# Kernel tuning notes

Hardware: AMD Instinct MI355X
Metric: run time of the kernel (lower is better)

The kernel has to match this reference:

```python
import jax, jax.numpy as jnp
import numpy as np

N_USER = 100_000
N_WALLET = 100_000
E = 1_600_000
HID, OUT = 128, 64
H, C = 4, 32  # GAT heads, per-head channels (HID // 4)
U_IN, W_IN = 16, 4
EPS = 1e-5


def _sage(x_src, x_dst, ei, w_l, b_l, w_r):
    """PyG SAGEConv (mean aggr): lin_l(mean_j x_j) + lin_r(x_i)."""
    src, dst = ei[0], ei[1]
    n = x_dst.shape[0]
    s = jax.ops.segment_sum(x_src[src], dst, num_segments=n)
    deg = jax.ops.segment_sum(jnp.ones((src.shape[0],), x_src.dtype), dst, num_segments=n)
    agg = s / jnp.maximum(deg, 1.0)[:, None]
    return agg @ w_l + b_l + x_dst @ w_r


def _bn(x, g, b):
    """BatchNorm over node dim (training-mode batch stats)."""
    m = x.mean(0)
    v = x.var(0)
    return (x - m) * jax.lax.rsqrt(v + EPS) * g + b


def _segment_softmax(logits, seg, n):
    m = jax.ops.segment_max(logits, seg, num_segments=n)
    e = jnp.exp(logits - m[seg])
    s = jax.ops.segment_sum(e, seg, num_segments=n)
    return e / (s[seg] + 1e-16)


def _gat(x, ei, w, a_src, a_dst, bias):
    """PyG GATConv with self-loops, heads concatenated. Dropout off (eval)."""
    n = x.shape[0]
    loop = jnp.arange(n, dtype=ei.dtype)
    src = jnp.concatenate([ei[0], loop])
    dst = jnp.concatenate([ei[1], loop])
    xp = (x @ w).reshape(n, H, C)                      # [n,H,C]
    al_s = (xp * a_src).sum(-1)                        # [n,H]
    al_d = (xp * a_dst).sum(-1)                        # [n,H]
    logits = jax.nn.leaky_relu(al_s[src] + al_d[dst], 0.2)  # [E+n,H]
    alpha = _segment_softmax(logits, dst, n)
    out = jax.ops.segment_sum(xp[src] * alpha[:, :, None], dst, num_segments=n)
    return out.reshape(n, H * C) + bias


def setup_inputs() -> dict:
    key = jax.random.key(0)
    ks = jax.random.split(key, 24)
    rn = lambda k, s, sc=0.05: jax.random.normal(k, s, jnp.float32) * sc
    ei = lambda k, n: jax.random.randint(k, (2, E), 0, n, jnp.int32)
    return {
        "x_user": rn(ks[0], (N_USER, U_IN), 1.0),
        "x_wallet": rn(ks[1], (N_WALLET, W_IN), 1.0),
        "w_u2w_l": rn(ks[2], (U_IN, HID)), "b_u2w": jnp.zeros((HID,), jnp.float32), "w_u2w_r": rn(ks[3], (W_IN, HID)),
        "w_w2u_l": rn(ks[4], (W_IN, HID)), "b_w2u": jnp.zeros((HID,), jnp.float32), "w_w2u_r": rn(ks[5], (U_IN, HID)),
        "w_u2u_l": rn(ks[6], (U_IN, HID)), "b_u2u": jnp.zeros((HID,), jnp.float32), "w_u2u_r": rn(ks[7], (U_IN, HID)),
        "bn_u_g": jnp.ones((HID,), jnp.float32), "bn_u_b": jnp.zeros((HID,), jnp.float32),
        "bn_w_g": jnp.ones((HID,), jnp.float32), "bn_w_b": jnp.zeros((HID,), jnp.float32),
        "gat_w": rn(ks[8], (HID, H * C)), "gat_as": rn(ks[9], (H, C)), "gat_ad": rn(ks[10], (H, C)),
        "gat_b": jnp.zeros((HID,), jnp.float32),
        "bn2_g": jnp.ones((HID,), jnp.float32), "bn2_b": jnp.zeros((HID,), jnp.float32),
        "proj_w": rn(ks[11], (HID, OUT)), "proj_b": jnp.zeros((OUT,), jnp.float32),
        "ei_uw": ei(ks[12], N_USER),   # src user -> dst wallet (both 100k)
        "ei_wu": ei(ks[13], N_WALLET),  # src wallet -> dst user
        "ei_uu": ei(ks[14], N_USER),
    }


def reference(x_user, x_wallet, w_u2w_l, b_u2w, w_u2w_r, w_w2u_l, b_w2u, w_w2u_r,
              w_u2u_l, b_u2u, w_u2u_r, bn_u_g, bn_u_b, bn_w_g, bn_w_b,
              gat_w, gat_as, gat_ad, gat_b, bn2_g, bn2_b, proj_w, proj_b,
              ei_uw, ei_wu, ei_uu):
    h_w_from_u = jax.nn.relu(_sage(x_user, x_wallet, ei_uw, w_u2w_l, b_u2w, w_u2w_r))
    h_u_from_w = jax.nn.relu(_sage(x_wallet, x_user, ei_wu, w_w2u_l, b_w2u, w_w2u_r))
    h_u_from_u = jax.nn.relu(_sage(x_user, x_user, ei_uu, w_u2u_l, b_u2u, w_u2u_r))
    h_user = _bn(h_u_from_w + h_u_from_u, bn_u_g, bn_u_b)
    _ = _bn(h_w_from_u, bn_w_g, bn_w_b)  # h_wallet: computed in torch module but unused in output
    h_user = jax.nn.relu(_gat(h_user, ei_uu, gat_w, gat_as, gat_ad, gat_b))
    h_user = _bn(h_user, bn2_g, bn2_b)
    return jax.nn.relu(h_user @ proj_w + proj_b)  # dropout = identity (eval)
```

## Files before the change

kernel.cpp:

```cpp
#include <hip/hip_runtime.h>
#include <hip/hip_bf16.h>
#include <cstdint>
#include <cstddef>

#define NN   100000
#define NE   1600000
#define CAP  48

#define NBKT 98
#define BSH  10
#define FB   48
#define BCAP 17408
#define ACHUNK 2048
#define NABLK 784
#define SUBSH 7

#define NTILES 1563
#define CH_BN 500

typedef __attribute__((ext_vector_type(8))) short short8;
typedef __attribute__((ext_vector_type(4))) float floatx4;

__device__ inline short f2bs(float x) {
    __hip_bfloat16 h = __float2bfloat16(x);
    return *reinterpret_cast<short*>(&h);
}
__device__ inline int pack2(float a, float b) {
    return ((int)(unsigned short)f2bs(b) << 16) | (unsigned short)f2bs(a);
}
__device__ inline float bflo(unsigned p) { return __uint_as_float(p << 16); }
__device__ inline float bfhi(unsigned p) { return __uint_as_float(p & 0xFFFF0000u); }

#define OFF_PRE   ((size_t)0)
#define OFF_BKTU  ((size_t)0)
#define OFF_BKTW  ((size_t)1705984)
#define OFF_XP    ((size_t)12800000)
#define OFF_COLU  ((size_t)19200000)
#define OFF_CNTU  ((size_t)25600000)
#define OFF_CNTW  ((size_t)25700000)
#define OFF_BCUR  ((size_t)25800000)
#define OFF_S1    ((size_t)25800256)
#define OFF_Q1    ((size_t)25800384)
#define OFF_S2    ((size_t)25800512)
#define OFF_Q2    ((size_t)25800640)
#define OFF_ALS   ((size_t)25801280)
#define OFF_ALD   ((size_t)26201280)
#define OFF_AGGU  ((size_t)26601280)
#define OFF_AGGW  ((size_t)28201280)
#define ZBASE     OFF_BCUR
#define ZFLOATS   ((size_t)768)

__global__ void __launch_bounds__(256) bin_edges(
    const int* __restrict__ ei_u, const int* __restrict__ ei_w,
    int* __restrict__ bcur_u, int* __restrict__ bkt_u,
    int* __restrict__ bcur_w, int* __restrict__ bkt_w) {
    const int* ei = blockIdx.y ? ei_w : ei_u;
    int* bcur = blockIdx.y ? bcur_w : bcur_u;
    int* bkt  = blockIdx.y ? bkt_w  : bkt_u;
    __shared__ int lcnt[NBKT];
    __shared__ int lbuf[NBKT * FB];
    for (int i = threadIdx.x; i < NBKT; i += 256) lcnt[i] = 0;
    __syncthreads();
    int base = blockIdx.x * ACHUNK;
    #pragma unroll
    for (int k = 0; k < ACHUNK / 256; k++) {
        int e = base + k * 256 + threadIdx.x;
        if (e < NE) {
            int src = ei[e], dst = ei[NE + e];
            int b = dst >> BSH;
            int pk = ((dst & ((1 << BSH) - 1)) << 17) | src;
            int pos = atomicAdd(&lcnt[b], 1);
            if (pos < FB) lbuf[b * FB + pos] = pk;
            else {
                int g = atomicAdd(&bcur[b], 1);
                if (g < BCAP) bkt[(size_t)b * BCAP + g] = pk;
            }
        }
    }
    __syncthreads();
    int wid = threadIdx.x >> 6, lane = threadIdx.x & 63;
    const int BPW = (NBKT + 3) / 4;
    int b0w = wid * BPW;
    int nb = NBKT - b0w; if (nb > BPW) nb = BPW;
    int myn = 0, myg = 0;
    if (lane < nb) {
        int c = lcnt[b0w + lane];
        myn = c < FB ? c : FB;
        if (myn > 0) myg = atomicAdd(&bcur[b0w + lane], myn);
    }
    for (int j = 0; j < nb; j++) {
        int n = __shfl(myn, j, 64);
        if (n == 0) continue;
        int g0 = __shfl(myg, j, 64);
        int b = b0w + j;
        if (lane < n) {
            int g = g0 + lane;
            if (g < BCAP) bkt[(size_t)b * BCAP + g] = lbuf[b * FB + lane];
        }
    }
}

__global__ void __launch_bounds__(256) csr_from_buckets(
    const int* __restrict__ bcur_u, const int* __restrict__ bkt_u,
    int* __restrict__ cntg_u, int* __restrict__ colg_u,
    const int* __restrict__ bcur_w, const int* __restrict__ bkt_w,
    int* __restrict__ cntg_w, int* __restrict__ colg_w) {
    const int* bcur = blockIdx.y ? bcur_w : bcur_u;
    const int* bkt  = blockIdx.y ? bkt_w  : bkt_u;
    int* cnt_g = blockIdx.y ? cntg_w : cntg_u;
    int* col_g = blockIdx.y ? colg_w : colg_u;
    int B = blockIdx.x >> 3, sub = blockIdx.x & 7;
    int node_base = (B << BSH) + (sub << SUBSH);
    if (node_base >= NN) return;
    __shared__ int cnt[128];
    __shared__ int col[128 * CAP];
    if (threadIdx.x < 128) cnt[threadIdx.x] = 0;
    __syncthreads();
    int n = bcur[B]; if (n > BCAP) n = BCAP;
    const int* bp = bkt + (size_t)B * BCAP;
    for (int i = threadIdx.x; i < n; i += 256) {
        int p = bp[i];
        int dlow = p >> 17;
        if ((dlow >> SUBSH) == sub) {
            int d = dlow & 127;
            int pos = atomicAdd(&cnt[d], 1);
            if (pos < CAP) col[d * CAP + pos] = p & 0x1FFFF;
        }
    }
    __syncthreads();
    int nn_here = NN - node_base; if (nn_here > 128) nn_here = 128;
    if (threadIdx.x < nn_here) cnt_g[node_base + threadIdx.x] = cnt[threadIdx.x];
    int total4 = nn_here * CAP / 4;
    const int4* cs = (const int4*)col;
    int4* cg = (int4*)(col_g + (size_t)node_base * CAP);
    for (int i = threadIdx.x; i < total4; i += 256) cg[i] = cs[i];
}

__global__ void __launch_bounds__(256) sage_gather(
    const float* __restrict__ xu, const float* __restrict__ xw,
    const int* __restrict__ cnt_u, const int* __restrict__ col_u,
    const int* __restrict__ cnt_w, const int* __restrict__ col_w,
    float* __restrict__ aggu, float* __restrict__ aggw) {
    int i = (blockIdx.x * 256 + threadIdx.x) >> 6;
    int lane = threadIdx.x & 63;

    int degu = cnt_u[i], degw = cnt_w[i];
    int nu = degu < CAP ? degu : CAP, nw = degw < CAP ? degw : CAP;
    int mycu = (lane < nu) ? col_u[(size_t)i * CAP + lane] : 0;
    int mycw = (lane < nw) ? col_w[(size_t)i * CAP + lane] : 0;

    float vu;
    {
        int j = lane >> 4, k = lane & 15;
        float v0 = 0.f, v1 = 0.f, v2 = 0.f, v3 = 0.f;
        int iters = (nu + 15) >> 4;
        for (int it = 0; it < iters; it++) {
            int bb = j + (it << 4);
            int s0 = __shfl(mycu, bb, 64);
            int s1 = __shfl(mycu, bb + 4, 64);
            int s2 = __shfl(mycu, bb + 8, 64);
            int s3 = __shfl(mycu, bb + 12, 64);
            float x0 = xu[(size_t)s0 * 16 + k];
            float x1 = xu[(size_t)s1 * 16 + k];
            float x2 = xu[(size_t)s2 * 16 + k];
            float x3 = xu[(size_t)s3 * 16 + k];
            if (bb < nu)      v0 += x0;
            if (bb + 4 < nu)  v1 += x1;
            if (bb + 8 < nu)  v2 += x2;
            if (bb + 12 < nu) v3 += x3;
        }
        float v = (v0 + v1) + (v2 + v3);
        v += __shfl_xor(v, 16, 64);
        v += __shfl_xor(v, 32, 64);
        vu = v;
    }
    float vw;
    {
        int j = lane >> 2, k = lane & 3;
        float v0 = 0.f, v1 = 0.f;
        int iters = (nw + 31) >> 5;
        for (int it = 0; it < iters; it++) {
            int b0 = j + (it << 5), b1 = b0 + 16;
            int s0 = __shfl(mycw, b0, 64);
            int s1 = __shfl(mycw, b1, 64);
            float x0 = xw[(size_t)s0 * 4 + k];
            float x1 = xw[(size_t)s1 * 4 + k];
            if (b0 < nw) v0 += x0;
            if (b1 < nw) v1 += x1;
        }
        float v = v0 + v1;
        v += __shfl_xor(v, 4, 64);
        v += __shfl_xor(v, 8, 64);
        v += __shfl_xor(v, 16, 64);
        v += __shfl_xor(v, 32, 64);
        vw = v;
    }
    float iu = 1.f / fmaxf((float)degu, 1.f);
    float iw = 1.f / fmaxf((float)degw, 1.f);
    if (lane < 16) aggu[(size_t)i * 16 + lane] = vu * iu;
    if (lane < 4)  aggw[(size_t)i * 4 + lane]  = vw * iw;
}

__global__ void __launch_bounds__(256, 2) sage_gemm(
    const float* __restrict__ aggu, const float* __restrict__ aggw,
    const float* __restrict__ xu,
    const float* __restrict__ wl_w2u, const float* __restrict__ b_w2u, const float* __restrict__ wr_w2u,
    const float* __restrict__ wl_u2u, const float* __restrict__ b_u2u, const float* __restrict__ wr_u2u,
    __hip_bfloat16* __restrict__ pre) {
    __shared__ short lw[16 * 64 * 8];
    __shared__ short la[64 * 136];
    int tid = threadIdx.x;
    for (int idx = tid; idx < 8192; idx += 256) {
        int mat = idx >> 12;
        int k = (idx >> 7) & 31, n = idx & 127;
        float w;
        if (mat == 0)
            w = (k < 4) ? wl_w2u[k * 128 + n] : (k < 20 ? wr_w2u[(k - 4) * 128 + n] : 0.f);
        else
            w = (k < 16) ? wl_u2u[k * 128 + n] : wr_u2u[(k - 16) * 128 + n];
        int t = n >> 4, l15 = n & 15, q = (k >> 3) & 3, j = k & 7;
        lw[((mat * 8 + t) * 64 + q * 16 + l15) * 8 + j] = f2bs(w);
    }
    __syncthreads();
    int wv = tid >> 6, lane = tid & 63;
    int quad = lane >> 4, l15 = lane & 15;
    short8 w1[8], w2[8];
    #pragma unroll
    for (int t = 0; t < 8; t++) {
        w1[t] = *(const short8*)&lw[(t * 64 + lane) * 8];
        w2[t] = *(const short8*)&lw[((8 + t) * 64 + lane) * 8];
    }
    float bw[8], bu[8];
    #pragma unroll
    for (int t = 0; t < 8; t++) {
        bw[t] = b_w2u[t * 16 + l15];
        bu[t] = b_u2u[t * 16 + l15];
    }
    for (int tile = blockIdx.x; tile < NTILES; tile += gridDim.x) {
        int nbase = tile * 64;
        __syncthreads();
        {
            int node = tid >> 2, p = tid & 3;
            int gn = nbase + node;
            float4 v = make_float4(0.f, 0.f, 0.f, 0.f);
            if (gn < NN) v = *(const float4*)&xu[(size_t)gn * 16 + 4 * p];
            int2 pk; pk.x = pack2(v.x, v.y); pk.y = pack2(v.z, v.w);
            *(int2*)&la[node * 136 + 4 + 4 * p] = pk;
            *(int2*)&la[node * 136 + 48 + 4 * p] = pk;
        }
        {
            int node = tid >> 2, p = tid & 3;
            int gn = nbase + node;
            float4 v = make_float4(0.f, 0.f, 0.f, 0.f);
            if (gn < NN) v = *(const float4*)&aggu[(size_t)gn * 16 + 4 * p];
            int2 pk; pk.x = pack2(v.x, v.y); pk.y = pack2(v.z, v.w);
            *(int2*)&la[node * 136 + 32 + 4 * p] = pk;
        }
        if (tid < 64) {
            int node = tid, gn = nbase + node;
            float4 v = make_float4(0.f, 0.f, 0.f, 0.f);
            if (gn < NN) v = *(const float4*)&aggw[(size_t)gn * 4];
            int2 pk; pk.x = pack2(v.x, v.y); pk.y = pack2(v.z, v.w);
            *(int2*)&la[node * 136 + 0] = pk;
            int2 z; z.x = 0; z.y = 0;
            *(int2*)&la[node * 136 + 20] = z;
            *(int2*)&la[node * 136 + 24] = z;
            *(int2*)&la[node * 136 + 28] = z;
        }
        __syncthreads();
        short8 af1 = *(const short8*)&la[(wv * 16 + l15) * 136 + quad * 8];
        short8 af2 = *(const short8*)&la[(wv * 16 + l15) * 136 + 32 + quad * 8];
        floatx4 acc1[8], acc2[8];
        #pragma unroll
        for (int t = 0; t < 8; t++) {
            acc1[t] = (floatx4){0.f, 0.f, 0.f, 0.f};
            acc2[t] = (floatx4){0.f, 0.f, 0.f, 0.f};
        }
        #pragma unroll
        for (int t = 0; t < 8; t++) {
            acc1[t] = __builtin_amdgcn_mfma_f32_16x16x32_bf16(af1, w1[t], acc1[t], 0, 0, 0);
            acc2[t] = __builtin_amdgcn_mfma_f32_16x16x32_bf16(af2, w2[t], acc2[t], 0, 0, 0);
        }
        __syncthreads();
        #pragma unroll
        for (int t = 0; t < 8; t++)
            #pragma unroll
            for (int r = 0; r < 4; r++) {
                float v1 = fmaxf(acc1[t][r] + bw[t], 0.f);
                float v2 = fmaxf(acc2[t][r] + bu[t], 0.f);
                la[(wv * 16 + quad * 4 + r) * 136 + t * 16 + l15] = f2bs(v1 + v2);
            }
        __syncthreads();
        #pragma unroll
        for (int c = 0; c < 4; c++) {
            int idx = c * 256 + tid;
            int node = idx >> 4, f8 = (idx & 15) * 8;
            int gn = nbase + node;
            if (gn < NN)
                *(int4*)(pre + (size_t)gn * 128 + f8) = *(const int4*)&la[node * 136 + f8];
        }
    }
}

__global__ void __launch_bounds__(256) bn_stats_pre2(const unsigned* __restrict__ x2,
                                                     float* __restrict__ sum, float* __restrict__ sq) {
    int f2 = threadIdx.x & 63, half = threadIdx.x >> 6;
    int n0 = blockIdx.x * CH_BN;
    float s0 = 0.f, q0 = 0.f, s1 = 0.f, q1 = 0.f;
    for (int i = n0 + half; i < n0 + CH_BN; i += 4) {
        unsigned p = x2[(size_t)i * 64 + f2];
        float v0 = bflo(p), v1 = bfhi(p);
        s0 += v0; q0 += v0 * v0; s1 += v1; q1 += v1 * v1;
    }
    __shared__ float a0[256], c0[256], a1[256], c1[256];
    a0[threadIdx.x] = s0; c0[threadIdx.x] = q0;
    a1[threadIdx.x] = s1; c1[threadIdx.x] = q1;
    __syncthreads();
    if (half == 0) {
        for (int h = 1; h < 4; h++) {
            s0 += a0[h * 64 + f2]; q0 += c0[h * 64 + f2];
            s1 += a1[h * 64 + f2]; q1 += c1[h * 64 + f2];
        }
        atomicAdd(&sum[2 * f2], s0);     atomicAdd(&sq[2 * f2], q0);
        atomicAdd(&sum[2 * f2 + 1], s1); atomicAdd(&sq[2 * f2 + 1], q1);
    }
}

__global__ void __launch_bounds__(256) bn_stats_act2(const unsigned* __restrict__ x2,
                                                     const float* __restrict__ gb,
                                                     float* __restrict__ sum, float* __restrict__ sq) {
    int f2 = threadIdx.x & 63, half = threadIdx.x >> 6;
    int n0 = blockIdx.x * CH_BN;
    float gb0 = gb[2 * f2], gb1 = gb[2 * f2 + 1];
    float s0 = 0.f, q0 = 0.f, s1 = 0.f, q1 = 0.f;
    for (int i = n0 + half; i < n0 + CH_BN; i += 4) {
        unsigned p = x2[(size_t)i * 64 + f2];
        float v0 = fmaxf(bflo(p) + gb0, 0.f), v1 = fmaxf(bfhi(p) + gb1, 0.f);
        s0 += v0; q0 += v0 * v0; s1 += v1; q1 += v1 * v1;
    }
    __shared__ float a0[256], c0[256], a1[256], c1[256];
    a0[threadIdx.x] = s0; c0[threadIdx.x] = q0;
    a1[threadIdx.x] = s1; c1[threadIdx.x] = q1;
    __syncthreads();
    if (half == 0) {
        for (int h = 1; h < 4; h++) {
            s0 += a0[h * 64 + f2]; q0 += c0[h * 64 + f2];
            s1 += a1[h * 64 + f2]; q1 += c1[h * 64 + f2];
        }
        atomicAdd(&sum[2 * f2], s0);     atomicAdd(&sq[2 * f2], q0);
        atomicAdd(&sum[2 * f2 + 1], s1); atomicAdd(&sq[2 * f2 + 1], q1);
    }
}

__global__ void __launch_bounds__(256, 2) gemm_al(
    const unsigned* __restrict__ pre2, const float* __restrict__ s1, const float* __restrict__ q1,
    const float* __restrict__ bng, const float* __restrict__ bnb,
    const float* __restrict__ gw, const float* __restrict__ gas, const float* __restrict__ gad,
    __hip_bfloat16* __restrict__ xp, float* __restrict__ al_s, float* __restrict__ al_d) {
    __shared__ short lw[32 * 64 * 8];
    __shared__ short la[64 * 136];
    __shared__ float lsc[128], lsh[128];
    int tid = threadIdx.x;
    if (tid < 128) {
        float m = s1[tid] * (1.0f / NN);
        float v = q1[tid] * (1.0f / NN) - m * m;
        float sc = bng[tid] * rsqrtf(v + 1e-5f);
        lsc[tid] = sc; lsh[tid] = bnb[tid] - m * sc;
    }
    for (int idx = tid; idx < 16384; idx += 256) {
        int k = idx >> 7, n = idx & 127;
        int t = n >> 4, l15 = n & 15, s = k >> 5, q = (k >> 3) & 3, j = k & 7;
        lw[(((t * 4 + s) * 64) + q * 16 + l15) * 8 + j] = f2bs(gw[idx]);
    }
    __syncthreads();
    int wv = tid >> 6, lane = tid & 63;
    int quad = lane >> 4, l15 = lane & 15;
    short8 wfrag[8][4];
    #pragma unroll
    for (int t = 0; t < 8; t++)
        #pragma unroll
        for (int s = 0; s < 4; s++)
            wfrag[t][s] = *(const short8*)&lw[((t * 4 + s) * 64 + lane) * 8];
    float asv[8], adv[8];
    #pragma unroll
    for (int t = 0; t < 8; t++) {
        asv[t] = gas[t * 16 + l15];
        adv[t] = gad[t * 16 + l15];
    }
    for (int tile = blockIdx.x; tile < NTILES; tile += gridDim.x) {
        int nbase = tile * 64;
        __syncthreads();
        #pragma unroll
        for (int c = 0; c < 8; c++) {
            int idx = c * 256 + tid;
            int node = idx >> 5, g = idx & 31;
            uint2 pp = make_uint2(0u, 0u);
            int gn = nbase + node;
            if (gn < NN) pp = *(const uint2*)&pre2[(size_t)gn * 64 + 2 * g];
            int f = 4 * g;
            float v0 = bflo(pp.x), v1 = bfhi(pp.x), v2 = bflo(pp.y), v3 = bfhi(pp.y);
            int2 pk;
            pk.x = pack2(v0 * lsc[f] + lsh[f],         v1 * lsc[f + 1] + lsh[f + 1]);
            pk.y = pack2(v2 * lsc[f + 2] + lsh[f + 2], v3 * lsc[f + 3] + lsh[f + 3]);
            *(int2*)&la[node * 136 + f] = pk;
        }
        __syncthreads();
        short8 af[4];
        #pragma unroll
        for (int s = 0; s < 4; s++)
            af[s] = *(const short8*)&la[(wv * 16 + l15) * 136 + s * 32 + quad * 8];
        floatx4 acc[8];
        #pragma unroll
        for (int t = 0; t < 8; t++) acc[t] = (floatx4){0.f, 0.f, 0.f, 0.f};
        #pragma unroll
        for (int s = 0; s < 4; s++)
            #pragma unroll
            for (int t = 0; t < 8; t++)
                acc[t] = __builtin_amdgcn_mfma_f32_16x16x32_bf16(af[s], wfrag[t][s], acc[t], 0, 0, 0);
        #pragma unroll
        for (int r = 0; r < 4; r++) {
            int node = nbase + wv * 16 + quad * 4 + r;
            #pragma unroll
            for (int h = 0; h < 4; h++) {
                float vs = acc[2 * h][r] * asv[2 * h] + acc[2 * h + 1][r] * asv[2 * h + 1];
                float vd = acc[2 * h][r] * adv[2 * h] + acc[2 * h + 1][r] * adv[2 * h + 1];
                #pragma unroll
                for (int m = 8; m >= 1; m >>= 1) {
                    vs += __shfl_xor(vs, m, 64);
                    vd += __shfl_xor(vd, m, 64);
                }
                if (l15 == 0 && node < NN) {
                    al_s[(size_t)node * 4 + h] = vs;
                    al_d[(size_t)node * 4 + h] = vd;
                }
            }
        }
        __syncthreads();
        #pragma unroll
        for (int t = 0; t < 8; t++)
            #pragma unroll
            for (int r = 0; r < 4; r++)
                la[(wv * 16 + quad * 4 + r) * 136 + t * 16 + l15] = f2bs(acc[t][r]);
        __syncthreads();
        #pragma unroll
        for (int c = 0; c < 4; c++) {
            int idx = c * 256 + tid;
            int node = idx >> 4, f8 = (idx & 15) * 8;
            int gn = nbase + node;
            if (gn < NN)
                *(int4*)(xp + (size_t)gn * 128 + f8) = *(const int4*)&la[node * 136 + f8];
        }
    }
}

__global__ void __launch_bounds__(256, 2) gemm_proj(
    const unsigned* __restrict__ gat2, const float* __restrict__ gb,
    const float* __restrict__ s2, const float* __restrict__ q2,
    const float* __restrict__ bng, const float* __restrict__ bnb,
    const float* __restrict__ pw, const float* __restrict__ pb,
    float* __restrict__ out) {
    __shared__ short lw[16 * 64 * 8];
    __shared__ short la[64 * 136];
    __shared__ float lsc[128], lsh[128], lgb[128];
    int tid = threadIdx.x;
    if (tid < 128) {
        float m = s2[tid] * (1.0f / NN);
        float v = q2[tid] * (1.0f / NN) - m * m;
        float sc = bng[tid] * rsqrtf(v + 1e-5f);
        lsc[tid] = sc; lsh[tid] = bnb[tid] - m * sc;
        lgb[tid] = gb[tid];
    }
    for (int idx = tid; idx < 8192; idx += 256) {
        int k = idx >> 6, n = idx & 63;
        int t = n >> 4, l15 = n & 15, s = k >> 5, q = (k >> 3) & 3, j = k & 7;
        lw[(((t * 4 + s) * 64) + q * 16 + l15) * 8 + j] = f2bs(pw[idx]);
    }
    __syncthreads();
    int wv = tid >> 6, lane = tid & 63;
    int quad = lane >> 4, l15 = lane & 15;
    short8 wfrag[4][4];
    #pragma unroll
    for (int t = 0; t < 4; t++)
        #pragma unroll
        for (int s = 0; s < 4; s++)
            wfrag[t][s] = *(const short8*)&lw[((t * 4 + s) * 64 + lane) * 8];
    float pbv[4];
    #pragma unroll
    for (int t = 0; t < 4; t++) pbv[t] = pb[t * 16 + l15];
    for (int tile = blockIdx.x; tile < NTILES; tile += gridDim.x) {
        int nbase = tile * 64;
        __syncthreads();
        #pragma unroll
        for (int c = 0; c < 8; c++) {
            int idx = c * 256 + tid;
            int node = idx >> 5, g = idx & 31;
            uint2 pp = make_uint2(0u, 0u);
            int gn = nbase + node;
            if (gn < NN) pp = *(const uint2*)&gat2[(size_t)gn * 64 + 2 * g];
            int f = 4 * g;
            float h0 = fmaxf(bflo(pp.x) + lgb[f],     0.f) * lsc[f]     + lsh[f];
            float h1 = fmaxf(bfhi(pp.x) + lgb[f + 1], 0.f) * lsc[f + 1] + lsh[f + 1];
            float h2 = fmaxf(bflo(pp.y) + lgb[f + 2], 0.f) * lsc[f + 2] + lsh[f + 2];
            float h3 = fmaxf(bfhi(pp.y) + lgb[f + 3], 0.f) * lsc[f + 3] + lsh[f + 3];
            int2 pk; pk.x = pack2(h0, h1); pk.y = pack2(h2, h3);
            *(int2*)&la[node * 136 + f] = pk;
        }
        __syncthreads();
        short8 af[4];
        #pragma unroll
        for (int s = 0; s < 4; s++)
            af[s] = *(const short8*)&la[(wv * 16 + l15) * 136 + s * 32 + quad * 8];
        floatx4 acc[4];
        #pragma unroll
        for (int t = 0; t < 4; t++) acc[t] = (floatx4){0.f, 0.f, 0.f, 0.f};
        #pragma unroll
        for (int s = 0; s < 4; s++)
            #pragma unroll
            for (int t = 0; t < 4; t++)
                acc[t] = __builtin_amdgcn_mfma_f32_16x16x32_bf16(af[s], wfrag[t][s], acc[t], 0, 0, 0);
        #pragma unroll
        for (int r = 0; r < 4; r++) {
            int gn = nbase + wv * 16 + quad * 4 + r;
            if (gn < NN) {
                #pragma unroll
                for (int t = 0; t < 4; t++)
                    out[(size_t)gn * 64 + t * 16 + l15] = fmaxf(acc[t][r] + pbv[t], 0.f);
            }
        }
    }
}

__global__ void __launch_bounds__(256) gat_gather(
    const int* __restrict__ cnt_u, const int* __restrict__ col_u,
    const float* __restrict__ al_s, const float* __restrict__ al_d,
    const unsigned* __restrict__ xp2, unsigned* __restrict__ gout2) {
    int i = (blockIdx.x * 256 + threadIdx.x) >> 6;
    int lane = threadIdx.x & 63;
    int h = lane >> 4;
    float ad = al_d[(size_t)i * 4 + h];
    int deg = cnt_u[i];
    int n = deg < CAP ? deg : CAP;
    int mycol = (lane < n) ? col_u[(size_t)i * CAP + lane] : 0;
    float l = al_s[(size_t)i * 4 + h] + ad; l = l > 0.f ? l : 0.2f * l;
    float e = __expf(l);
    unsigned p = xp2[(size_t)i * 64 + lane];
    float acc0 = e * bflo(p), acc1 = e * bfhi(p), den = e;
    int b = 0;
    for (; b + 4 <= n; b += 4) {
        int s0 = __shfl(mycol, b, 64);
        int s1 = __shfl(mycol, b + 1, 64);
        int s2 = __shfl(mycol, b + 2, 64);
        int s3 = __shfl(mycol, b + 3, 64);
        float a0 = al_s[(size_t)s0 * 4 + h];
        float a1 = al_s[(size_t)s1 * 4 + h];
        float a2 = al_s[(size_t)s2 * 4 + h];
        float a3 = al_s[(size_t)s3 * 4 + h];
        unsigned p0 = xp2[(size_t)s0 * 64 + lane];
        unsigned p1 = xp2[(size_t)s1 * 64 + lane];
        unsigned p2 = xp2[(size_t)s2 * 64 + lane];
        unsigned p3 = xp2[(size_t)s3 * 64 + lane];
        float l0 = a0 + ad; l0 = l0 > 0.f ? l0 : 0.2f * l0;
        float l1 = a1 + ad; l1 = l1 > 0.f ? l1 : 0.2f * l1;
        float l2 = a2 + ad; l2 = l2 > 0.f ? l2 : 0.2f * l2;
        float l3 = a3 + ad; l3 = l3 > 0.f ? l3 : 0.2f * l3;
        float e0 = __expf(l0), e1 = __expf(l1), e2 = __expf(l2), e3 = __expf(l3);
        acc0 += e0 * bflo(p0) + e1 * bflo(p1) + e2 * bflo(p2) + e3 * bflo(p3);
        acc1 += e0 * bfhi(p0) + e1 * bfhi(p1) + e2 * bfhi(p2) + e3 * bfhi(p3);
        den  += e0 + e1 + e2 + e3;
    }
    for (; b < n; b++) {
        int s = __shfl(mycol, b, 64);
        float a = al_s[(size_t)s * 4 + h];
        unsigned pp = xp2[(size_t)s * 64 + lane];
        float ll = a + ad; ll = ll > 0.f ? ll : 0.2f * ll;
        float ee = __expf(ll);
        acc0 += ee * bflo(pp);
        acc1 += ee * bfhi(pp);
        den += ee;
    }
    float r = 1.0f / (den + 1e-16f);
    gout2[(size_t)i * 64 + lane] = (unsigned)pack2(acc0 * r, acc1 * r);
}

extern "C" void kernel_launch(void* const* d_in, const int* in_sizes, int n_in,
                              void* d_out, int out_size, void* d_ws, size_t ws_size,
                              hipStream_t stream) {
    const float* x_user   = (const float*)d_in[0];
    const float* x_wallet = (const float*)d_in[1];
    const float* w_w2u_l  = (const float*)d_in[5];
    const float* b_w2u    = (const float*)d_in[6];
    const float* w_w2u_r  = (const float*)d_in[7];
    const float* w_u2u_l  = (const float*)d_in[8];
    const float* b_u2u    = (const float*)d_in[9];
    const float* w_u2u_r  = (const float*)d_in[10];
    const float* bn_u_g   = (const float*)d_in[11];
    const float* bn_u_b   = (const float*)d_in[12];
    const float* gat_w    = (const float*)d_in[15];
    const float* gat_as   = (const float*)d_in[16];
    const float* gat_ad   = (const float*)d_in[17];
    const float* gat_b    = (const float*)d_in[18];
    const float* bn2_g    = (const float*)d_in[19];
    const float* bn2_b    = (const float*)d_in[20];
    const float* proj_w   = (const float*)d_in[21];
    const float* proj_b   = (const float*)d_in[22];
    const int* ei_wu      = (const int*)d_in[24];
    const int* ei_uu      = (const int*)d_in[25];
    float* out = (float*)d_out;
    float* ws  = (float*)d_ws;

    __hip_bfloat16* pre = (__hip_bfloat16*)(ws + OFF_PRE);
    unsigned* pre2 = (unsigned*)(ws + OFF_PRE);
    int*   bkt_u  = (int*)(ws + OFF_BKTU);
    int*   bkt_w  = (int*)(ws + OFF_BKTW);
    __hip_bfloat16* xp = (__hip_bfloat16*)(ws + OFF_XP);
    unsigned* xp2 = (unsigned*)(ws + OFF_XP);
    int*   col_w  = (int*)(ws + OFF_XP);
    int*   col_u  = (int*)(ws + OFF_COLU);
    int*   cnt_u  = (int*)(ws + OFF_CNTU);
    int*   cnt_w  = (int*)(ws + OFF_CNTW);
    int*   bcur_u = (int*)(ws + OFF_BCUR);
    int*   bcur_w = (int*)(ws + OFF_BCUR) + 128;
    float* al_s = ws + OFF_ALS, *al_d = ws + OFF_ALD;
    float* s1 = ws + OFF_S1, *q1 = ws + OFF_Q1;
    float* s2 = ws + OFF_S2, *q2 = ws + OFF_Q2;
    float* aggu = ws + OFF_AGGU, *aggw = ws + OFF_AGGW;

    hipMemsetAsync(ws + ZBASE, 0, ZFLOATS * sizeof(float), stream);

    bin_edges<<<dim3(NABLK, 2), 256, 0, stream>>>(ei_uu, ei_wu, bcur_u, bkt_u, bcur_w, bkt_w);
    csr_from_buckets<<<dim3(NBKT * 8, 2), 256, 0, stream>>>(
        bcur_u, bkt_u, cnt_u, col_u, bcur_w, bkt_w, cnt_w, col_w);

    sage_gather<<<NN / 4, 256, 0, stream>>>(
        x_user, x_wallet, cnt_u, col_u, cnt_w, col_w, aggu, aggw);

    sage_gemm<<<512, 256, 0, stream>>>(
        aggu, aggw, x_user, w_w2u_l, b_w2u, w_w2u_r, w_u2u_l, b_u2u, w_u2u_r, pre);

    bn_stats_pre2<<<NN / CH_BN, 256, 0, stream>>>(pre2, s1, q1);

    gemm_al<<<512, 256, 0, stream>>>(pre2, s1, q1, bn_u_g, bn_u_b,
                                     gat_w, gat_as, gat_ad, xp, al_s, al_d);

    unsigned* gat2 = pre2;
    gat_gather<<<NN / 4, 256, 0, stream>>>(cnt_u, col_u, al_s, al_d, xp2, gat2);

    bn_stats_act2<<<NN / CH_BN, 256, 0, stream>>>(gat2, gat_b, s2, q2);

    gemm_proj<<<512, 256, 0, stream>>>(gat2, gat_b, s2, q2, bn2_g, bn2_b,
                                       proj_w, proj_b, out);
}
```

Measured before the change: 495.0 us.

## Fuse CSR construction with SAGE mean aggregation and use exp2 in GAT softmax

Merges the CSR-building kernel and the SAGE neighbour gather into one kernel that aggregates directly from the CSR columns held in shared memory. The wallet CSR no longer has to be written to or re-read from global memory, and one launch is removed. The GAT attention vectors are pre-scaled by log2(e) so the gather can use exp2f with a max-based leaky ReLU. The cost is less parallelism in the aggregation: each wave now walks 32 nodes serially.

```diff
diff --git a/kernel.cpp b/kernel.cpp
--- a/kernel.cpp
+++ b/kernel.cpp
@@ -17,6 +17,7 @@
 
 #define NTILES 1563
 #define CH_BN 500
+#define LOG2E 1.44269504088896f
 
 typedef __attribute__((ext_vector_type(8))) short short8;
 typedef __attribute__((ext_vector_type(4))) float floatx4;
@@ -37,7 +38,6 @@
 #define OFF_XP    ((size_t)12800000)
 #define OFF_COLU  ((size_t)19200000)
 #define OFF_CNTU  ((size_t)25600000)
-#define OFF_CNTW  ((size_t)25700000)
 #define OFF_BCUR  ((size_t)25800000)
 #define OFF_S1    ((size_t)25800256)
 #define OFF_Q1    ((size_t)25800384)
@@ -100,15 +100,15 @@
     }
 }
 
-__global__ void __launch_bounds__(256) csr_from_buckets(
+__global__ void __launch_bounds__(256) csr_agg(
     const int* __restrict__ bcur_u, const int* __restrict__ bkt_u,
-    int* __restrict__ cntg_u, int* __restrict__ colg_u,
+    int* __restrict__ cnt_g, int* __restrict__ col_g,
+    const float* __restrict__ xu, float* __restrict__ aggu,
     const int* __restrict__ bcur_w, const int* __restrict__ bkt_w,
-    int* __restrict__ cntg_w, int* __restrict__ colg_w) {
-    const int* bcur = blockIdx.y ? bcur_w : bcur_u;
-    const int* bkt  = blockIdx.y ? bkt_w  : bkt_u;
-    int* cnt_g = blockIdx.y ? cntg_w : cntg_u;
-    int* col_g = blockIdx.y ? colg_w : colg_u;
+    const float* __restrict__ xw, float* __restrict__ aggw) {
+    int type = blockIdx.y;
+    const int* bcur = type ? bcur_w : bcur_u;
+    const int* bkt  = type ? bkt_w  : bkt_u;
     int B = blockIdx.x >> 3, sub = blockIdx.x & 7;
     int node_base = (B << BSH) + (sub << SUBSH);
     if (node_base >= NN) return;
@@ -129,76 +129,62 @@
     }
     __syncthreads();
     int nn_here = NN - node_base; if (nn_here > 128) nn_here = 128;
-    if (threadIdx.x < nn_here) cnt_g[node_base + threadIdx.x] = cnt[threadIdx.x];
-    int total4 = nn_here * CAP / 4;
-    const int4* cs = (const int4*)col;
-    int4* cg = (int4*)(col_g + (size_t)node_base * CAP);
-    for (int i = threadIdx.x; i < total4; i += 256) cg[i] = cs[i];
-}
-
-__global__ void __launch_bounds__(256) sage_gather(
-    const float* __restrict__ xu, const float* __restrict__ xw,
-    const int* __restrict__ cnt_u, const int* __restrict__ col_u,
-    const int* __restrict__ cnt_w, const int* __restrict__ col_w,
-    float* __restrict__ aggu, float* __restrict__ aggw) {
-    int i = (blockIdx.x * 256 + threadIdx.x) >> 6;
-    int lane = threadIdx.x & 63;
-
-    int degu = cnt_u[i], degw = cnt_w[i];
-    int nu = degu < CAP ? degu : CAP, nw = degw < CAP ? degw : CAP;
-    int mycu = (lane < nu) ? col_u[(size_t)i * CAP + lane] : 0;
-    int mycw = (lane < nw) ? col_w[(size_t)i * CAP + lane] : 0;
-
-    float vu;
-    {
+    int wv = threadIdx.x >> 6, lane = threadIdx.x & 63;
+
+    if (type == 0) {
+        if (threadIdx.x < nn_here) cnt_g[node_base + threadIdx.x] = cnt[threadIdx.x];
+        int total4 = nn_here * CAP / 4;
+        const int4* cs = (const int4*)col;
+        int4* cg = (int4*)(col_g + (size_t)node_base * CAP);
+        for (int i = threadIdx.x; i < total4; i += 256) cg[i] = cs[i];
         int j = lane >> 4, k = lane & 15;
-        float v0 = 0.f, v1 = 0.f, v2 = 0.f, v3 = 0.f;
-        int iters = (nu + 15) >> 4;
-        for (int it = 0; it < iters; it++) {
-            int bb = j + (it << 4);
-            int s0 = __shfl(mycu, bb, 64);
-            int s1 = __shfl(mycu, bb + 4, 64);
-            int s2 = __shfl(mycu, bb + 8, 64);
-            int s3 = __shfl(mycu, bb + 12, 64);
-            float x0 = xu[(size_t)s0 * 16 + k];
-            float x1 = xu[(size_t)s1 * 16 + k];
-            float x2 = xu[(size_t)s2 * 16 + k];
-            float x3 = xu[(size_t)s3 * 16 + k];
-            if (bb < nu)      v0 += x0;
-            if (bb + 4 < nu)  v1 += x1;
-            if (bb + 8 < nu)  v2 += x2;
-            if (bb + 12 < nu) v3 += x3;
-        }
-        float v = (v0 + v1) + (v2 + v3);
-        v += __shfl_xor(v, 16, 64);
-        v += __shfl_xor(v, 32, 64);
-        vu = v;
-    }
-    float vw;
-    {
+        for (int nl = wv * 32; nl < wv * 32 + 32 && nl < nn_here; nl++) {
+            int deg = cnt[nl];
+            int nu = deg < CAP ? deg : CAP;
+            float v0 = 0.f, v1 = 0.f, v2 = 0.f, v3 = 0.f;
+            int iters = (nu + 15) >> 4;
+            for (int it = 0; it < iters; it++) {
+                int bb = j + (it << 4);
+                int s0 = (bb < nu)      ? col[nl * CAP + bb]      : 0;
+                int s1 = (bb + 4 < nu)  ? col[nl * CAP + bb + 4]  : 0;
+                int s2 = (bb + 8 < nu)  ? col[nl * CAP + bb + 8]  : 0;
+                int s3 = (bb + 12 < nu) ? col[nl * CAP + bb + 12] : 0;
+                float x0 = xu[(size_t)s0 * 16 + k];
+                float x1 = xu[(size_t)s1 * 16 + k];
+                float x2 = xu[(size_t)s2 * 16 + k];
+                float x3 = xu[(size_t)s3 * 16 + k];
+                if (bb < nu)      v0 += x0;
+                if (bb + 4 < nu)  v1 += x1;
+                if (bb + 8 < nu)  v2 += x2;
+                if (bb + 12 < nu) v3 += x3;
+            }
+            float v = (v0 + v1) + (v2 + v3);
+            v += __shfl_xor(v, 16, 64);
+            v += __shfl_xor(v, 32, 64);
+            if (lane < 16)
+                aggu[(size_t)(node_base + nl) * 16 + lane] = v / fmaxf((float)deg, 1.f);
+        }
+    } else {
         int j = lane >> 2, k = lane & 3;
-        float v0 = 0.f, v1 = 0.f;
-        int iters = (nw + 31) >> 5;
-        for (int it = 0; it < iters; it++) {
-            int b0 = j + (it << 5), b1 = b0 + 16;
-            int s0 = __shfl(mycw, b0, 64);
-            int s1 = __shfl(mycw, b1, 64);
-            float x0 = xw[(size_t)s0 * 4 + k];
-            float x1 = xw[(size_t)s1 * 4 + k];
-            if (b0 < nw) v0 += x0;
-            if (b1 < nw) v1 += x1;
-        }
-        float v = v0 + v1;
-        v += __shfl_xor(v, 4, 64);
-        v += __shfl_xor(v, 8, 64);
-        v += __shfl_xor(v, 16, 64);
-        v += __shfl_xor(v, 32, 64);
-        vw = v;
-    }
-    float iu = 1.f / fmaxf((float)degu, 1.f);
-    float iw = 1.f / fmaxf((float)degw, 1.f);
-    if (lane < 16) aggu[(size_t)i * 16 + lane] = vu * iu;
-    if (lane < 4)  aggw[(size_t)i * 4 + lane]  = vw * iw;
+        for (int nl = wv * 32; nl < wv * 32 + 32 && nl < nn_here; nl++) {
+            int deg = cnt[nl];
+            int nw = deg < CAP ? deg : CAP;
+            float v = 0.f;
+            int iters = (nw + 15) >> 4;
+            for (int it = 0; it < iters; it++) {
+                int bb = j + (it << 4);
+                int s = (bb < nw) ? col[nl * CAP + bb] : 0;
+                float x = xw[(size_t)s * 4 + k];
+                if (bb < nw) v += x;
+            }
+            v += __shfl_xor(v, 4, 64);
+            v += __shfl_xor(v, 8, 64);
+            v += __shfl_xor(v, 16, 64);
+            v += __shfl_xor(v, 32, 64);
+            if (lane < 4)
+                aggw[(size_t)(node_base + nl) * 4 + lane] = v / fmaxf((float)deg, 1.f);
+        }
+    }
 }
 
 __global__ void __launch_bounds__(256, 2) sage_gemm(
@@ -384,8 +370,8 @@
     float asv[8], adv[8];
     #pragma unroll
     for (int t = 0; t < 8; t++) {
-        asv[t] = gas[t * 16 + l15];
-        adv[t] = gad[t * 16 + l15];
+        asv[t] = gas[t * 16 + l15] * LOG2E;
+        adv[t] = gad[t * 16 + l15] * LOG2E;
     }
     for (int tile = blockIdx.x; tile < NTILES; tile += gridDim.x) {
         int nbase = tile * 64;
@@ -541,8 +527,8 @@
     int deg = cnt_u[i];
     int n = deg < CAP ? deg : CAP;
     int mycol = (lane < n) ? col_u[(size_t)i * CAP + lane] : 0;
-    float l = al_s[(size_t)i * 4 + h] + ad; l = l > 0.f ? l : 0.2f * l;
-    float e = __expf(l);
+    float l = al_s[(size_t)i * 4 + h] + ad;
+    float e = exp2f(fmaxf(l, 0.2f * l));
     unsigned p = xp2[(size_t)i * 64 + lane];
     float acc0 = e * bflo(p), acc1 = e * bfhi(p), den = e;
     int b = 0;
@@ -559,11 +545,11 @@
         unsigned p1 = xp2[(size_t)s1 * 64 + lane];
         unsigned p2 = xp2[(size_t)s2 * 64 + lane];
         unsigned p3 = xp2[(size_t)s3 * 64 + lane];
-        float l0 = a0 + ad; l0 = l0 > 0.f ? l0 : 0.2f * l0;
-        float l1 = a1 + ad; l1 = l1 > 0.f ? l1 : 0.2f * l1;
-        float l2 = a2 + ad; l2 = l2 > 0.f ? l2 : 0.2f * l2;
-        float l3 = a3 + ad; l3 = l3 > 0.f ? l3 : 0.2f * l3;
-        float e0 = __expf(l0), e1 = __expf(l1), e2 = __expf(l2), e3 = __expf(l3);
+        float l0 = a0 + ad, l1 = a1 + ad, l2 = a2 + ad, l3 = a3 + ad;
+        float e0 = exp2f(fmaxf(l0, 0.2f * l0));
+        float e1 = exp2f(fmaxf(l1, 0.2f * l1));
+        float e2 = exp2f(fmaxf(l2, 0.2f * l2));
+        float e3 = exp2f(fmaxf(l3, 0.2f * l3));
         acc0 += e0 * bflo(p0) + e1 * bflo(p1) + e2 * bflo(p2) + e3 * bflo(p3);
         acc1 += e0 * bfhi(p0) + e1 * bfhi(p1) + e2 * bfhi(p2) + e3 * bfhi(p3);
         den  += e0 + e1 + e2 + e3;
@@ -572,8 +558,8 @@
         int s = __shfl(mycol, b, 64);
         float a = al_s[(size_t)s * 4 + h];
         unsigned pp = xp2[(size_t)s * 64 + lane];
-        float ll = a + ad; ll = ll > 0.f ? ll : 0.2f * ll;
-        float ee = __expf(ll);
+        float ll = a + ad;
+        float ee = exp2f(fmaxf(ll, 0.2f * ll));
         acc0 += ee * bflo(pp);
         acc1 += ee * bfhi(pp);
         den += ee;
@@ -608,16 +594,14 @@
     float* out = (float*)d_out;
     float* ws  = (float*)d_ws;
 
+    unsigned* pre2 = (unsigned*)(ws + OFF_PRE);
     __hip_bfloat16* pre = (__hip_bfloat16*)(ws + OFF_PRE);
-    unsigned* pre2 = (unsigned*)(ws + OFF_PRE);
     int*   bkt_u  = (int*)(ws + OFF_BKTU);
     int*   bkt_w  = (int*)(ws + OFF_BKTW);
     __hip_bfloat16* xp = (__hip_bfloat16*)(ws + OFF_XP);
     unsigned* xp2 = (unsigned*)(ws + OFF_XP);
-    int*   col_w  = (int*)(ws + OFF_XP);
     int*   col_u  = (int*)(ws + OFF_COLU);
     int*   cnt_u  = (int*)(ws + OFF_CNTU);
-    int*   cnt_w  = (int*)(ws + OFF_CNTW);
     int*   bcur_u = (int*)(ws + OFF_BCUR);
     int*   bcur_w = (int*)(ws + OFF_BCUR) + 128;
     float* al_s = ws + OFF_ALS, *al_d = ws + OFF_ALD;
@@ -628,11 +612,10 @@
     hipMemsetAsync(ws + ZBASE, 0, ZFLOATS * sizeof(float), stream);
 
     bin_edges<<<dim3(NABLK, 2), 256, 0, stream>>>(ei_uu, ei_wu, bcur_u, bkt_u, bcur_w, bkt_w);
-    csr_from_buckets<<<dim3(NBKT * 8, 2), 256, 0, stream>>>(
-        bcur_u, bkt_u, cnt_u, col_u, bcur_w, bkt_w, cnt_w, col_w);
-
-    sage_gather<<<NN / 4, 256, 0, stream>>>(
-        x_user, x_wallet, cnt_u, col_u, cnt_w, col_w, aggu, aggw);
+
+    csr_agg<<<dim3(NBKT * 8, 2), 256, 0, stream>>>(
+        bcur_u, bkt_u, cnt_u, col_u, x_user, aggu,
+        bcur_w, bkt_w, x_wallet, aggw);
 
     sage_gemm<<<512, 256, 0, stream>>>(
         aggu, aggw, x_user, w_w2u_l, b_w2u, w_w2u_r, w_u2u_l, b_u2u, w_u2u_r, pre);
```

Measured after the change: 513.9 us. 3.8% more time.
